# Performance work log

Measured on AMD Instinct MI355X. Metric: run time of the kernel, lower is better.

Reference implementation:

```python
import jax, jax.numpy as jnp
import numpy as np

# FP4 (E2M1) code table: nibble = [sign(1) | exp(2) | mantissa(1)]
# magnitudes for codes 0..7: 0, 0.5, 1, 1.5, 2, 3, 4, 6; codes 8..15 are negated.
_MAG = np.array([0.0, 0.5, 1.0, 1.5, 2.0, 3.0, 4.0, 6.0], dtype=np.float32)
FP4_LUT = jnp.asarray(np.concatenate([_MAG, -_MAG]))  # [16]

BLOCK = 16  # scale-factor block size along in_features


def setup_inputs() -> dict:
    key = jax.random.key(0)
    k0, k1, k2, k3, k4 = jax.random.split(key, 5)
    M, K, N = 32, 8192, 8192  # tokens, in_features, out_features
    inp = jax.random.normal(k0, (M, K), dtype=jnp.float32)
    qweight = jax.random.randint(k1, (N, K // 2), 0, 256, dtype=jnp.int32)  # packed FP4 pairs
    scales = jax.random.uniform(k2, (N, K // BLOCK), dtype=jnp.float32)      # per-block scales
    amax = jax.random.uniform(k3, (1,), dtype=jnp.float32) + 0.5             # global scale
    bias = jax.random.normal(k4, (N,), dtype=jnp.float32)
    return {"input": inp, "qweight": qweight, "scales": scales, "amax": amax, "bias": bias}


def _dequantize(qweight, scales, amax):
    N = qweight.shape[0]
    low = qweight & 0xF            # first element of each pair
    high = (qweight >> 4) & 0xF    # second element
    nibbles = jnp.stack([low, high], axis=-1).reshape(N, -1)  # [N, K]
    vals = FP4_LUT[nibbles]                                   # [N, K] fp4 values
    # per-block scaling: block of BLOCK contiguous in-features shares one scale
    w = (vals.reshape(N, -1, BLOCK) * scales[..., None]).reshape(N, -1)
    return w * amax[0]


def reference(input, qweight, scales, amax, bias):
    weight = _dequantize(qweight, scales, amax)   # [N, K] full-precision weight
    return input @ weight.T + bias                # F.linear
```

## Files before the change

### kernel.cpp

```cpp
#include <hip/hip_runtime.h>
#include <hip/hip_bf16.h>

#define M_DIM 32
#define K_DIM 8192
#define N_DIM 8192
#define KS 16
#define KCH (K_DIM / KS)
#define CHK 128
#define NCHK (KCH / CHK)
#define STEPS (CHK / 32)
#define NPB 64
#define MAIN_BLOCKS ((N_DIM / NPB) * KS)

#define QW_ROWI4 (K_DIM / 8)
#define SC_ROW (K_DIM / 16)

#define QROW 17
#define AROW 136
#define SROW 9

typedef _Float16 half8   __attribute__((ext_vector_type(8)));
typedef _Float16 half4_t __attribute__((ext_vector_type(4)));
typedef float    floatx4 __attribute__((ext_vector_type(4)));
typedef float    floatx2 __attribute__((ext_vector_type(2)));

__device__ __forceinline__ uint32_t dec2(uint32_t b) {
  uint32_t c0 = b & 0xFu, c1 = (b >> 4) & 0xFu;
  uint32_t m0 = c0 & 7u, m1 = c1 & 7u;
  uint32_t t0 = min(28u * m0, m0 + 28u);
  uint32_t t1 = min(28u * m1, m1 + 28u);
  return (t0 << 9) | ((c0 & 8u) << 12)
       | (t1 << 25) | ((c1 & 8u) << 28);
}

__device__ __forceinline__ half8 decode8p(uint32_t q, _Float16 s) {
  union { uint32_t u[4]; half8 h; } w;
  w.u[0] = dec2(q & 0xFFu);
  w.u[1] = dec2((q >> 8) & 0xFFu);
  w.u[2] = dec2((q >> 16) & 0xFFu);
  w.u[3] = dec2((q >> 24) & 0xFFu);
  half8 sv = {s, s, s, s, s, s, s, s};
  return w.h * sv;
}

__global__ void convertA_kernel(const floatx4* __restrict__ in4,
                                half4_t* __restrict__ out4) {
  int idx = blockIdx.x * blockDim.x + threadIdx.x;
  floatx4 f = in4[idx];
  half4_t h;
  h[0] = (_Float16)f[0]; h[1] = (_Float16)f[1];
  h[2] = (_Float16)f[2]; h[3] = (_Float16)f[3];
  out4[idx] = h;
}

__global__ void reduce_kernel(const floatx4* __restrict__ part,
                              const floatx4* __restrict__ bias4,
                              floatx4* __restrict__ out4) {
  int idx = blockIdx.x * blockDim.x + threadIdx.x;
  floatx4 acc = bias4[idx & (N_DIM / 4 - 1)];
#pragma unroll
  for (int s = 0; s < KS; ++s)
    acc += part[(size_t)s * (M_DIM * N_DIM / 4) + idx];
  out4[idx] = acc;
}

template <bool F16A>
__global__ __launch_bounds__(256, 4) void fp4_linear_kernel(
    const void*  __restrict__ Av,
    const int4*  __restrict__ qw4,
    const float* __restrict__ scales,
    const float* __restrict__ amaxp,
    float*       __restrict__ part)
{
  __shared__ uint32_t Qs[NPB * QROW];
  __shared__ _Float16 As[M_DIM * AROW];
  __shared__ float    Ss[NPB * SROW];

  const int t    = threadIdx.x;
  const int lane = t & 63;
  const int w    = t >> 6;
  const int ks   = blockIdx.x & (KS - 1);
  const int nb   = blockIdx.x >> 4;
  const int n0   = nb * NPB;
  const int kb   = ks * KCH;
  const float amax = amaxp[0];

  const int qr = t >> 4, qc = t & 15;
  const int4* qsrc = qw4 + (size_t)(n0 + qr) * QW_ROWI4 + ks * (KCH / 8) + qc;
  const int sr = t >> 2, sh = t & 3;
  const float* ssrc = scales + (size_t)(n0 + sr) * SC_ROW + ks * (KCH / 16) + sh * 2;
  const int ar16 = t >> 4, ac16 = t & 15;
  const _Float16* asrc16 =
      (const _Float16*)Av + (size_t)ar16 * K_DIM + kb + ac16 * 8;
  const int ar32 = t >> 5, ac32 = t & 31;
  const float* asrc32 = (const float*)Av + (size_t)ar32 * K_DIM + kb + ac32 * 4;

  int4    qreg[4];
  half8   areg16[2];
  floatx4 areg32[4];
  floatx2 sreg;

  {
#pragma unroll
    for (int j = 0; j < 4; ++j)
      qreg[j] = qsrc[(size_t)j * 16 * QW_ROWI4];
    if (F16A) {
#pragma unroll
      for (int j = 0; j < 2; ++j)
        areg16[j] = *(const half8*)(asrc16 + (size_t)j * 16 * K_DIM);
    } else {
#pragma unroll
      for (int j = 0; j < 4; ++j)
        areg32[j] = *(const floatx4*)(asrc32 + (size_t)j * 8 * K_DIM);
    }
    sreg = *(const floatx2*)ssrc;
  }

  const int row  = lane & 15;
  const int quad = lane >> 4;
  const int nloc = w * 16;
  const uint32_t* qAp = &Qs[(nloc + row) * QROW];
  const _Float16* a0p = &As[row * AROW];
  const _Float16* a1p = &As[(row + 16) * AROW];
  const float*    sAp = &Ss[(nloc + row) * SROW];

  floatx4 acc0 = {0.f, 0.f, 0.f, 0.f};
  floatx4 acc1 = {0.f, 0.f, 0.f, 0.f};

  for (int c = 0; c < NCHK; ++c) {
    if (c) __syncthreads();

#pragma unroll
    for (int j = 0; j < 4; ++j) {
      uint32_t pk = ((uint32_t)qreg[j].x & 0xFFu)
                  | (((uint32_t)qreg[j].y & 0xFFu) << 8)
                  | (((uint32_t)qreg[j].z & 0xFFu) << 16)
                  | (((uint32_t)qreg[j].w & 0xFFu) << 24);
      Qs[(j * 16 + qr) * QROW + qc] = pk;
    }
    if (F16A) {
#pragma unroll
      for (int j = 0; j < 2; ++j)
        *(half8*)&As[(j * 16 + ar16) * AROW + ac16 * 8] = areg16[j];
    } else {
#pragma unroll
      for (int j = 0; j < 4; ++j) {
        floatx4 f = areg32[j];
        half4_t h;
        h[0] = (_Float16)f[0]; h[1] = (_Float16)f[1];
        h[2] = (_Float16)f[2]; h[3] = (_Float16)f[3];
        *(half4_t*)&As[(j * 8 + ar32) * AROW + ac32 * 4] = h;
      }
    }
    {
      float* sd = &Ss[sr * SROW + sh * 2];
      sd[0] = sreg[0] * amax; sd[1] = sreg[1] * amax;
    }
    __syncthreads();

    if (c + 1 < NCHK) {
      const int co = c + 1;
#pragma unroll
      for (int j = 0; j < 4; ++j)
        qreg[j] = qsrc[(size_t)j * 16 * QW_ROWI4 + co * (CHK / 8)];
      if (F16A) {
#pragma unroll
        for (int j = 0; j < 2; ++j)
          areg16[j] = *(const half8*)(asrc16 + (size_t)j * 16 * K_DIM + co * CHK);
      } else {
#pragma unroll
        for (int j = 0; j < 4; ++j)
          areg32[j] = *(const floatx4*)(asrc32 + (size_t)j * 8 * K_DIM + co * CHK);
      }
      sreg = *(const floatx2*)(ssrc + co * (CHK / 16));
    }

#pragma unroll
    for (int it = 0; it < STEPS; ++it) {
      const uint32_t qA = qAp[it * 4 + quad];
      const _Float16 sA = (_Float16)sAp[it * 2 + (quad >> 1)];
      half8 bA = decode8p(qA, sA);
      half8 a0 = *(const half8*)(a0p + it * 32 + quad * 8);
      half8 a1 = *(const half8*)(a1p + it * 32 + quad * 8);
      acc0 = __builtin_amdgcn_mfma_f32_16x16x32_f16(a0, bA, acc0, 0, 0, 0);
      acc1 = __builtin_amdgcn_mfma_f32_16x16x32_f16(a1, bA, acc1, 0, 0, 0);
    }
  }

  float* pb = part + (size_t)ks * (M_DIM * N_DIM);
#pragma unroll
  for (int r = 0; r < 4; ++r) {
    const int m = quad * 4 + r;
    float* o0 = pb + (size_t)m * N_DIM + n0 + nloc;
    float* o1 = pb + (size_t)(m + 16) * N_DIM + n0 + nloc;
    o0[row] = acc0[r];
    o1[row] = acc1[r];
  }
}

extern "C" void kernel_launch(void* const* d_in, const int* in_sizes, int n_in,
                              void* d_out, int out_size, void* d_ws, size_t ws_size,
                              hipStream_t stream) {
  const float* inp    = (const float*)d_in[0];
  const int4*  qw4    = (const int4*)d_in[1];
  const float* scales = (const float*)d_in[2];
  const float* amaxp  = (const float*)d_in[3];
  const float* bias   = (const float*)d_in[4];
  float* out = (float*)d_out;

  const size_t part_bytes = (size_t)KS * M_DIM * N_DIM * sizeof(float);
  const size_t a16_bytes  = (size_t)M_DIM * K_DIM * sizeof(_Float16);
  float* partp = (float*)d_ws;

  if (ws_size >= part_bytes + a16_bytes) {
    _Float16* Af16 = (_Float16*)((char*)d_ws + part_bytes);
    convertA_kernel<<<M_DIM * K_DIM / 4 / 256, 256, 0, stream>>>(
        (const floatx4*)inp, (half4_t*)Af16);
    fp4_linear_kernel<true><<<MAIN_BLOCKS, 256, 0, stream>>>(
        Af16, qw4, scales, amaxp, partp);
  } else {
    fp4_linear_kernel<false><<<MAIN_BLOCKS, 256, 0, stream>>>(
        inp, qw4, scales, amaxp, partp);
  }
  reduce_kernel<<<M_DIM * N_DIM / 4 / 256, 256, 0, stream>>>(
      (const floatx4*)partp, (const floatx4*)bias, (floatx4*)out);
}
```

Measured before the change: 222.4 us.

## Replace split-K partial buffer and reduce kernel with atomic accumulation

The split-K reduction pass is removed. A prep kernel now initializes the output with bias and converts the activations to fp16 in a single launch, and the main kernel atomically adds its partial tiles straight into the output. The split-K factor is halved, so there are half as many blocks, each doing twice the K range. This drops the partial-buffer writes and reads plus one launch, but adds float atomics, which make summation order nondeterministic, and it reduces the block count available for parallelism.

```diff
diff --git a/kernel.cpp b/kernel.cpp
--- a/kernel.cpp
+++ b/kernel.cpp
@@ -4,7 +4,7 @@
 #define M_DIM 32
 #define K_DIM 8192
 #define N_DIM 8192
-#define KS 16
+#define KS 8
 #define KCH (K_DIM / KS)
 #define CHK 128
 #define NCHK (KCH / CHK)
@@ -43,25 +43,22 @@
   return w.h * sv;
 }
 
-__global__ void convertA_kernel(const floatx4* __restrict__ in4,
-                                half4_t* __restrict__ out4) {
-  int idx = blockIdx.x * blockDim.x + threadIdx.x;
-  floatx4 f = in4[idx];
-  half4_t h;
-  h[0] = (_Float16)f[0]; h[1] = (_Float16)f[1];
-  h[2] = (_Float16)f[2]; h[3] = (_Float16)f[3];
-  out4[idx] = h;
-}
-
-__global__ void reduce_kernel(const floatx4* __restrict__ part,
-                              const floatx4* __restrict__ bias4,
-                              floatx4* __restrict__ out4) {
-  int idx = blockIdx.x * blockDim.x + threadIdx.x;
-  floatx4 acc = bias4[idx & (N_DIM / 4 - 1)];
-#pragma unroll
-  for (int s = 0; s < KS; ++s)
-    acc += part[(size_t)s * (M_DIM * N_DIM / 4) + idx];
-  out4[idx] = acc;
+__global__ void prep_kernel(const floatx4* __restrict__ in4,
+                            half4_t* __restrict__ a16,
+                            const floatx4* __restrict__ bias4,
+                            floatx4* __restrict__ out4) {
+  int b = blockIdx.x;
+  if (b < (M_DIM * N_DIM / 4 / 256)) {
+    int idx = b * 256 + threadIdx.x;
+    out4[idx] = bias4[idx & (N_DIM / 4 - 1)];
+  } else {
+    int idx = (b - (M_DIM * N_DIM / 4 / 256)) * 256 + threadIdx.x;
+    floatx4 f = in4[idx];
+    half4_t h;
+    h[0] = (_Float16)f[0]; h[1] = (_Float16)f[1];
+    h[2] = (_Float16)f[2]; h[3] = (_Float16)f[3];
+    a16[idx] = h;
+  }
 }
 
 template <bool F16A>
@@ -70,7 +67,7 @@
     const int4*  __restrict__ qw4,
     const float* __restrict__ scales,
     const float* __restrict__ amaxp,
-    float*       __restrict__ part)
+    float*       __restrict__ out)
 {
   __shared__ uint32_t Qs[NPB * QROW];
   __shared__ _Float16 As[M_DIM * AROW];
@@ -80,7 +77,7 @@
   const int lane = t & 63;
   const int w    = t >> 6;
   const int ks   = blockIdx.x & (KS - 1);
-  const int nb   = blockIdx.x >> 4;
+  const int nb   = blockIdx.x >> 3;
   const int n0   = nb * NPB;
   const int kb   = ks * KCH;
   const float amax = amaxp[0];
@@ -187,14 +184,11 @@
     }
   }
 
-  float* pb = part + (size_t)ks * (M_DIM * N_DIM);
 #pragma unroll
   for (int r = 0; r < 4; ++r) {
     const int m = quad * 4 + r;
-    float* o0 = pb + (size_t)m * N_DIM + n0 + nloc;
-    float* o1 = pb + (size_t)(m + 16) * N_DIM + n0 + nloc;
-    o0[row] = acc0[r];
-    o1[row] = acc1[r];
+    atomicAdd(&out[(size_t)m * N_DIM + n0 + nloc + row], acc0[r]);
+    atomicAdd(&out[(size_t)(m + 16) * N_DIM + n0 + nloc + row], acc1[r]);
   }
 }
 
@@ -208,20 +202,21 @@
   const float* bias   = (const float*)d_in[4];
   float* out = (float*)d_out;
 
-  const size_t part_bytes = (size_t)KS * M_DIM * N_DIM * sizeof(float);
-  const size_t a16_bytes  = (size_t)M_DIM * K_DIM * sizeof(_Float16);
-  float* partp = (float*)d_ws;
-
-  if (ws_size >= part_bytes + a16_bytes) {
-    _Float16* Af16 = (_Float16*)((char*)d_ws + part_bytes);
-    convertA_kernel<<<M_DIM * K_DIM / 4 / 256, 256, 0, stream>>>(
-        (const floatx4*)inp, (half4_t*)Af16);
+  const size_t a16_bytes = (size_t)M_DIM * K_DIM * sizeof(_Float16);
+  const int init_blocks = M_DIM * N_DIM / 4 / 256;
+  const int conv_blocks = M_DIM * K_DIM / 4 / 256;
+
+  if (ws_size >= a16_bytes) {
+    _Float16* Af16 = (_Float16*)d_ws;
+    prep_kernel<<<init_blocks + conv_blocks, 256, 0, stream>>>(
+        (const floatx4*)inp, (half4_t*)Af16, (const floatx4*)bias,
+        (floatx4*)out);
     fp4_linear_kernel<true><<<MAIN_BLOCKS, 256, 0, stream>>>(
-        Af16, qw4, scales, amaxp, partp);
+        Af16, qw4, scales, amaxp, out);
   } else {
+    prep_kernel<<<init_blocks, 256, 0, stream>>>(
+        nullptr, nullptr, (const floatx4*)bias, (floatx4*)out);
     fp4_linear_kernel<false><<<MAIN_BLOCKS, 256, 0, stream>>>(
-        inp, qw4, scales, amaxp, partp);
-  }
-  reduce_kernel<<<M_DIM * N_DIM / 4 / 256, 256, 0, stream>>>(
-      (const floatx4*)partp, (const floatx4*)bias, (floatx4*)out);
-}
+        inp, qw4, scales, amaxp, out);
+  }
+}
```

Result: faster. 214.9 us (-3.4%).
